# Performance work log

Measured on AMD Instinct MI355X. Metric: run time of the kernel, lower is better.

## Reference

```python
import jax, jax.numpy as jnp
import numpy as np

Q_DIM = 512
K_DIM = 512
V_DIM = 512
H_DIM = 256
B, Q, K = 4, 512, 512


def setup_inputs() -> dict:
    key = jax.random.key(0)
    ks = jax.random.split(key, 7)
    q = jax.random.normal(ks[0], (B, Q, Q_DIM), dtype=jnp.float32)
    k = jax.random.normal(ks[1], (B, K, K_DIM), dtype=jnp.float32)
    v = jax.random.normal(ks[2], (B, K, V_DIM), dtype=jnp.float32)
    S = jax.random.randint(ks[3], (B,), 1, K + 1, dtype=jnp.int64)
    # learned params (nn.Linear stores weight of shape (out, in); y = x @ W.T)
    Wq = jax.random.normal(ks[4], (H_DIM, Q_DIM), dtype=jnp.float32) / np.sqrt(Q_DIM)
    Wk = jax.random.normal(ks[5], (H_DIM, K_DIM), dtype=jnp.float32) / np.sqrt(K_DIM)
    w = jax.random.normal(ks[6], (H_DIM,), dtype=jnp.float32) / np.sqrt(H_DIM)
    return {"q": q, "k": k, "v": v, "S": S, "Wq": Wq, "Wk": Wk, "w": w}


def reference(q, k, v, S, Wq, Wk, w):
    # Additive (Bahdanau) attention scores.
    pq = jnp.einsum('bqd,hd->bqh', q, Wq)            # (B, Q, H)
    pk = jnp.einsum('bkd,hd->bkh', k, Wk)            # (B, K, H)
    t = jnp.tanh(pq[:, :, None, :] + pk[:, None, :, :])  # (B, Q, K, H)
    scores = jnp.einsum('bqkh,h->bqk', t, w)         # (B, Q, K)
    # mask keys with index >= S[b] to -inf
    kv_idx = jnp.arange(scores.shape[-1])            # (K,)
    mask = kv_idx[None, None, :] >= S[:, None, None] # (B, 1, K) -> broadcast
    scores = jnp.where(mask, -jnp.inf, scores)
    return scores
```

## Files before the change

### kernel.cpp

```cpp
#include <hip/hip_runtime.h>
#include <hip/hip_bf16.h>
#include <math.h>

#define QDIM 512
#define HDIM 256
#define QQ 512
#define KKE 512

#define TWO_LOG2E 2.8853900817779268f
#define MASK_VAL -1.0e30f

typedef __attribute__((ext_vector_type(8))) short bf16x8;
typedef __attribute__((ext_vector_type(4))) float f32x4;

__device__ __forceinline__ unsigned int pk2(float x, float y) {
  __hip_bfloat162 h = __float22bfloat162_rn(make_float2(x, y));
  unsigned int u;
  __builtin_memcpy(&u, &h, 4);
  return u;
}

__global__ __launch_bounds__(512) void proj_kernel(
    const float* __restrict__ qin, const float* __restrict__ kin,
    const float* __restrict__ Wq, const float* __restrict__ Wk,
    const float* __restrict__ wvec,
    float* __restrict__ EqT, unsigned short* __restrict__ EkT,
    float* __restrict__ wsum_out) {
  __shared__ __align__(16) unsigned short As[32 * 72];
  __shared__ __align__(16) unsigned short Bs[64 * 72];

  const int tid = threadIdx.x;
  const int lane = tid & 63;
  const int wv = __builtin_amdgcn_readfirstlane(tid >> 6);
  const int quad = lane >> 4;
  const int l16 = lane & 15;

  const int m0 = blockIdx.x * 32;
  const int h0 = blockIdx.y * 64;
  const bool isk = (blockIdx.z != 0);
  const float* A = isk ? kin : qin;
  const float* W = isk ? Wk : Wq;

  const int srow = tid >> 4;
  const int sg = (tid & 15) * 4;

  const float* arow_g = &A[(size_t)(m0 + srow) * QDIM + sg];
  const float* brow0_g = &W[(size_t)(h0 + srow) * QDIM + sg];
  const float* brow1_g = &W[(size_t)(h0 + srow + 32) * QDIM + sg];
  unsigned short* adst = &As[srow * 72 + sg];
  unsigned short* bdst0 = &Bs[srow * 72 + sg];
  unsigned short* bdst1 = &Bs[(srow + 32) * 72 + sg];

  const unsigned short* afrag = &As[((wv & 1) * 16 + l16) * 72 + quad * 8];
  const unsigned short* bfrag = &Bs[((wv >> 1) * 16 + l16) * 72 + quad * 8];

  f32x4 acc = (f32x4){0.f, 0.f, 0.f, 0.f};

  float4 pa = *(const float4*)arow_g;
  float4 pb0 = *(const float4*)brow0_g;
  float4 pb1 = *(const float4*)brow1_g;

  for (int kc = 0; kc < QDIM; kc += 64) {
    __syncthreads();
    *(uint2*)adst = make_uint2(pk2(pa.x, pa.y), pk2(pa.z, pa.w));
    *(uint2*)bdst0 = make_uint2(pk2(pb0.x, pb0.y), pk2(pb0.z, pb0.w));
    *(uint2*)bdst1 = make_uint2(pk2(pb1.x, pb1.y), pk2(pb1.z, pb1.w));
    if (kc + 64 < QDIM) {
      pa = *(const float4*)(arow_g + kc + 64);
      pb0 = *(const float4*)(brow0_g + kc + 64);
      pb1 = *(const float4*)(brow1_g + kc + 64);
    }
    __syncthreads();
    bf16x8 a0 = *(const bf16x8*)afrag;
    bf16x8 a1 = *(const bf16x8*)(afrag + 32);
    bf16x8 b0 = *(const bf16x8*)bfrag;
    bf16x8 b1 = *(const bf16x8*)(bfrag + 32);
    acc = __builtin_amdgcn_mfma_f32_16x16x32_bf16(a0, b0, acc, 0, 0, 0);
    acc = __builtin_amdgcn_mfma_f32_16x16x32_bf16(a1, b1, acc, 0, 0, 0);
  }

  const int b = m0 >> 9;
  const int hrow = h0 + (wv >> 1) * 16 + l16;
  const int mcol = (m0 & 511) + (wv & 1) * 16 + quad * 4;
  float e0 = __builtin_amdgcn_exp2f(acc[0] * TWO_LOG2E);
  float e1 = __builtin_amdgcn_exp2f(acc[1] * TWO_LOG2E);
  float e2 = __builtin_amdgcn_exp2f(acc[2] * TWO_LOG2E);
  float e3 = __builtin_amdgcn_exp2f(acc[3] * TWO_LOG2E);
  if (!isk) {
    *(float4*)(EqT + ((size_t)b * HDIM + hrow) * 512 + mcol) =
        make_float4(e0, e1, e2, e3);
    if (m0 == 0 && h0 == 0 && tid < 64) {
      float s = wvec[tid] + wvec[tid + 64] + wvec[tid + 128] + wvec[tid + 192];
#pragma unroll
      for (int off = 32; off; off >>= 1) s += __shfl_down(s, off);
      if (tid == 0) wsum_out[0] = s;
    }
  } else {
    *(uint2*)(EkT + ((size_t)b * HDIM + hrow) * 512 + mcol) =
        make_uint2(pk2(e0, e1), pk2(e2, e3));
  }
}

__global__ __launch_bounds__(256) void score_kernel(
    const float* __restrict__ EqT, const unsigned short* __restrict__ EkT,
    const float* __restrict__ wvec, const float* __restrict__ wsump,
    const int* __restrict__ Sraw, float* __restrict__ out) {
  const int b = blockIdx.z;
  const int q0 = blockIdx.y * 16;
  const int i = blockIdx.x;
  const int S = (Sraw[1] == 0) ? Sraw[2 * b] : Sraw[b];
  const int tid = threadIdx.x;
  const int wv = __builtin_amdgcn_readfirstlane(tid >> 6);
  const int L = tid & 63;
  const int q = L >> 2;
  const int k8 = (L & 3) * 8;

  __shared__ float wl[HDIM];
  __shared__ float Eqs[256][16];
  __shared__ unsigned short Eks[256][32];
  __shared__ float Cmb[3][64][8];
  wl[tid] = wvec[tid];

  const float wsum = wsump[0];
  const float* EqB = EqT + (size_t)b * (HDIM * QQ) + q0;
  const unsigned short* EkB0 = EkT + (size_t)b * (HDIM * KKE);

#pragma unroll
  for (int t = 0; t < 2; ++t) {
    const int kt = t ? (15 - i) : i;
    const int k0 = kt * 32;
    float* orow = out + ((size_t)(b * QQ + q0 + q) * KKE + k0 + k8);

    if (k0 >= S) {
      if (wv == 0) {
        float4 m4 = make_float4(MASK_VAL, MASK_VAL, MASK_VAL, MASK_VAL);
        *(float4*)&orow[0] = m4;
        *(float4*)&orow[4] = m4;
      }
      continue;
    }

    __syncthreads();
    {
      const unsigned short* EkB = EkB0 + k0;
      const int hr = tid >> 2;
      const int cq = (tid & 3) * 4;
      const int ce = (tid & 3) * 8;
#pragma unroll
      for (int p = 0; p < 4; p++) {
        *(float4*)&Eqs[hr + p * 64][cq] =
            *(const float4*)&EqB[(size_t)(hr + p * 64) * QQ + cq];
        *(uint4*)&Eks[hr + p * 64][ce] =
            *(const uint4*)&EkB[(size_t)(hr + p * 64) * KKE + ce];
      }
    }
    __syncthreads();

    float a0 = 0.f, a1 = 0.f, a2 = 0.f, a3 = 0.f;
    float a4 = 0.f, a5 = 0.f, a6 = 0.f, a7 = 0.f;
    const int hbase = wv * 64;
#pragma unroll 4
    for (int hh = 0; hh < 64; hh++) {
      const int h = hbase + hh;
      float wh = wl[h];
      float eq = Eqs[h][q];
      uint4 u = *(const uint4*)&Eks[h][k8];
      float e0 = __uint_as_float(u.x << 16);
      float e1 = __uint_as_float(u.x & 0xffff0000u);
      float e2 = __uint_as_float(u.y << 16);
      float e3 = __uint_as_float(u.y & 0xffff0000u);
      float e4 = __uint_as_float(u.z << 16);
      float e5 = __uint_as_float(u.z & 0xffff0000u);
      float e6 = __uint_as_float(u.w << 16);
      float e7 = __uint_as_float(u.w & 0xffff0000u);
      a0 = fmaf(wh, __builtin_amdgcn_rcpf(fmaf(eq, e0, 1.f)), a0);
      a1 = fmaf(wh, __builtin_amdgcn_rcpf(fmaf(eq, e1, 1.f)), a1);
      a2 = fmaf(wh, __builtin_amdgcn_rcpf(fmaf(eq, e2, 1.f)), a2);
      a3 = fmaf(wh, __builtin_amdgcn_rcpf(fmaf(eq, e3, 1.f)), a3);
      a4 = fmaf(wh, __builtin_amdgcn_rcpf(fmaf(eq, e4, 1.f)), a4);
      a5 = fmaf(wh, __builtin_amdgcn_rcpf(fmaf(eq, e5, 1.f)), a5);
      a6 = fmaf(wh, __builtin_amdgcn_rcpf(fmaf(eq, e6, 1.f)), a6);
      a7 = fmaf(wh, __builtin_amdgcn_rcpf(fmaf(eq, e7, 1.f)), a7);
    }

    if (wv > 0) {
      Cmb[wv - 1][L][0] = a0; Cmb[wv - 1][L][1] = a1;
      Cmb[wv - 1][L][2] = a2; Cmb[wv - 1][L][3] = a3;
      Cmb[wv - 1][L][4] = a4; Cmb[wv - 1][L][5] = a5;
      Cmb[wv - 1][L][6] = a6; Cmb[wv - 1][L][7] = a7;
    }
    __syncthreads();
    if (wv == 0) {
#pragma unroll
      for (int c = 0; c < 3; c++) {
        a0 += Cmb[c][L][0]; a1 += Cmb[c][L][1];
        a2 += Cmb[c][L][2]; a3 += Cmb[c][L][3];
        a4 += Cmb[c][L][4]; a5 += Cmb[c][L][5];
        a6 += Cmb[c][L][6]; a7 += Cmb[c][L][7];
      }
      const int kb = k0 + k8;
      float4 r0, r1;
      r0.x = (kb + 0 < S) ? (wsum - 2.f * a0) : MASK_VAL;
      r0.y = (kb + 1 < S) ? (wsum - 2.f * a1) : MASK_VAL;
      r0.z = (kb + 2 < S) ? (wsum - 2.f * a2) : MASK_VAL;
      r0.w = (kb + 3 < S) ? (wsum - 2.f * a3) : MASK_VAL;
      r1.x = (kb + 4 < S) ? (wsum - 2.f * a4) : MASK_VAL;
      r1.y = (kb + 5 < S) ? (wsum - 2.f * a5) : MASK_VAL;
      r1.z = (kb + 6 < S) ? (wsum - 2.f * a6) : MASK_VAL;
      r1.w = (kb + 7 < S) ? (wsum - 2.f * a7) : MASK_VAL;
      *(float4*)&orow[0] = r0;
      *(float4*)&orow[4] = r1;
    }
  }
}

extern "C" void kernel_launch(void* const* d_in, const int* in_sizes, int n_in,
                              void* d_out, int out_size, void* d_ws, size_t ws_size,
                              hipStream_t stream) {
  const float* q  = (const float*)d_in[0];
  const float* k  = (const float*)d_in[1];
  const int*   S  = (const int*)d_in[3];
  const float* Wq = (const float*)d_in[4];
  const float* Wk = (const float*)d_in[5];
  const float* w  = (const float*)d_in[6];
  float* out = (float*)d_out;

  float* wsf = (float*)d_ws;
  float* EqT = wsf;
  unsigned short* EkT = (unsigned short*)(wsf + 524288);
  float* wsum = wsf + 524288 + 262144;

  proj_kernel<<<dim3(64, 4, 2), 512, 0, stream>>>(q, k, Wq, Wk, w, EqT, EkT, wsum);
  score_kernel<<<dim3(8, 32, 4), 256, 0, stream>>>(EqT, EkT, w, wsum, S, out);
}
```

Measured before the change: 97.82 us.

## Double-buffer projection LDS tiles and hoist Eq tile load in score kernel

Result: no change. 98.35 us (+0.5%).

```diff
diff --git a/kernel.cpp b/kernel.cpp
--- a/kernel.cpp
+++ b/kernel.cpp
@@ -26,8 +26,8 @@
     const float* __restrict__ wvec,
     float* __restrict__ EqT, unsigned short* __restrict__ EkT,
     float* __restrict__ wsum_out) {
-  __shared__ __align__(16) unsigned short As[32 * 72];
-  __shared__ __align__(16) unsigned short Bs[64 * 72];
+  __shared__ __align__(16) unsigned short As[2][32 * 72];
+  __shared__ __align__(16) unsigned short Bs[2][64 * 72];
 
   const int tid = threadIdx.x;
   const int lane = tid & 63;
@@ -47,36 +47,44 @@
   const float* arow_g = &A[(size_t)(m0 + srow) * QDIM + sg];
   const float* brow0_g = &W[(size_t)(h0 + srow) * QDIM + sg];
   const float* brow1_g = &W[(size_t)(h0 + srow + 32) * QDIM + sg];
-  unsigned short* adst = &As[srow * 72 + sg];
-  unsigned short* bdst0 = &Bs[srow * 72 + sg];
-  unsigned short* bdst1 = &Bs[(srow + 32) * 72 + sg];
-
-  const unsigned short* afrag = &As[((wv & 1) * 16 + l16) * 72 + quad * 8];
-  const unsigned short* bfrag = &Bs[((wv >> 1) * 16 + l16) * 72 + quad * 8];
+  const int adst = srow * 72 + sg;
+  const int bdst0 = srow * 72 + sg;
+  const int bdst1 = (srow + 32) * 72 + sg;
+
+  const int afo = ((wv & 1) * 16 + l16) * 72 + quad * 8;
+  const int bfo = ((wv >> 1) * 16 + l16) * 72 + quad * 8;
 
   f32x4 acc = (f32x4){0.f, 0.f, 0.f, 0.f};
 
   float4 pa = *(const float4*)arow_g;
   float4 pb0 = *(const float4*)brow0_g;
   float4 pb1 = *(const float4*)brow1_g;
-
+  *(uint2*)&As[0][adst] = make_uint2(pk2(pa.x, pa.y), pk2(pa.z, pa.w));
+  *(uint2*)&Bs[0][bdst0] = make_uint2(pk2(pb0.x, pb0.y), pk2(pb0.z, pb0.w));
+  *(uint2*)&Bs[0][bdst1] = make_uint2(pk2(pb1.x, pb1.y), pk2(pb1.z, pb1.w));
+  __syncthreads();
+
+#pragma unroll
   for (int kc = 0; kc < QDIM; kc += 64) {
-    __syncthreads();
-    *(uint2*)adst = make_uint2(pk2(pa.x, pa.y), pk2(pa.z, pa.w));
-    *(uint2*)bdst0 = make_uint2(pk2(pb0.x, pb0.y), pk2(pb0.z, pb0.w));
-    *(uint2*)bdst1 = make_uint2(pk2(pb1.x, pb1.y), pk2(pb1.z, pb1.w));
-    if (kc + 64 < QDIM) {
+    const int p = (kc >> 6) & 1;
+    const bool more = (kc + 64 < QDIM);
+    if (more) {
       pa = *(const float4*)(arow_g + kc + 64);
       pb0 = *(const float4*)(brow0_g + kc + 64);
       pb1 = *(const float4*)(brow1_g + kc + 64);
     }
-    __syncthreads();
-    bf16x8 a0 = *(const bf16x8*)afrag;
-    bf16x8 a1 = *(const bf16x8*)(afrag + 32);
-    bf16x8 b0 = *(const bf16x8*)bfrag;
-    bf16x8 b1 = *(const bf16x8*)(bfrag + 32);
+    bf16x8 a0 = *(const bf16x8*)&As[p][afo];
+    bf16x8 a1 = *(const bf16x8*)&As[p][afo + 32];
+    bf16x8 b0 = *(const bf16x8*)&Bs[p][bfo];
+    bf16x8 b1 = *(const bf16x8*)&Bs[p][bfo + 32];
     acc = __builtin_amdgcn_mfma_f32_16x16x32_bf16(a0, b0, acc, 0, 0, 0);
     acc = __builtin_amdgcn_mfma_f32_16x16x32_bf16(a1, b1, acc, 0, 0, 0);
+    if (more) {
+      *(uint2*)&As[p ^ 1][adst] = make_uint2(pk2(pa.x, pa.y), pk2(pa.z, pa.w));
+      *(uint2*)&Bs[p ^ 1][bdst0] = make_uint2(pk2(pb0.x, pb0.y), pk2(pb0.z, pb0.w));
+      *(uint2*)&Bs[p ^ 1][bdst1] = make_uint2(pk2(pb1.x, pb1.y), pk2(pb1.z, pb1.w));
+    }
+    __syncthreads();
   }
 
   const int b = m0 >> 9;
@@ -101,7 +109,7 @@
   }
 }
 
-__global__ __launch_bounds__(256) void score_kernel(
+__global__ __launch_bounds__(256, 4) void score_kernel(
     const float* __restrict__ EqT, const unsigned short* __restrict__ EkT,
     const float* __restrict__ wvec, const float* __restrict__ wsump,
     const int* __restrict__ Sraw, float* __restrict__ out) {
@@ -115,54 +123,51 @@
   const int q = L >> 2;
   const int k8 = (L & 3) * 8;
 
-  __shared__ float wl[HDIM];
-  __shared__ float Eqs[256][16];
-  __shared__ unsigned short Eks[256][32];
+  __shared__ float Eqs[HDIM][16];
+  __shared__ unsigned short Eks[HDIM][32];
   __shared__ float Cmb[3][64][8];
-  wl[tid] = wvec[tid];
-
+
+  {
+    const float* src = EqT + ((size_t)b * HDIM + tid) * QQ + q0;
+    *(float4*)&Eqs[tid][0] = *(const float4*)(src + 0);
+    *(float4*)&Eqs[tid][4] = *(const float4*)(src + 4);
+    *(float4*)&Eqs[tid][8] = *(const float4*)(src + 8);
+    *(float4*)&Eqs[tid][12] = *(const float4*)(src + 12);
+  }
   const float wsum = wsump[0];
-  const float* EqB = EqT + (size_t)b * (HDIM * QQ) + q0;
-  const unsigned short* EkB0 = EkT + (size_t)b * (HDIM * KKE);
+  const unsigned short* EkB = EkT + (size_t)b * (HDIM * KKE);
+  const int hbase = wv * 64;
 
 #pragma unroll
   for (int t = 0; t < 2; ++t) {
-    const int kt = t ? (15 - i) : i;
-    const int k0 = kt * 32;
-    float* orow = out + ((size_t)(b * QQ + q0 + q) * KKE + k0 + k8);
+    const int k0 = (t ? (15 - i) : i) * 32;
+    float* op = out + ((size_t)(b * QQ + q0 + q) * KKE + k0 + k8);
 
     if (k0 >= S) {
       if (wv == 0) {
         float4 m4 = make_float4(MASK_VAL, MASK_VAL, MASK_VAL, MASK_VAL);
-        *(float4*)&orow[0] = m4;
-        *(float4*)&orow[4] = m4;
+        *(float4*)&op[0] = m4;
+        *(float4*)&op[4] = m4;
       }
       continue;
     }
 
     __syncthreads();
     {
-      const unsigned short* EkB = EkB0 + k0;
-      const int hr = tid >> 2;
-      const int cq = (tid & 3) * 4;
-      const int ce = (tid & 3) * 8;
-#pragma unroll
-      for (int p = 0; p < 4; p++) {
-        *(float4*)&Eqs[hr + p * 64][cq] =
-            *(const float4*)&EqB[(size_t)(hr + p * 64) * QQ + cq];
-        *(uint4*)&Eks[hr + p * 64][ce] =
-            *(const uint4*)&EkB[(size_t)(hr + p * 64) * KKE + ce];
-      }
+      const unsigned short* sk = EkB + (size_t)tid * KKE + k0;
+      *(uint4*)&Eks[tid][0] = *(const uint4*)(sk + 0);
+      *(uint4*)&Eks[tid][8] = *(const uint4*)(sk + 8);
+      *(uint4*)&Eks[tid][16] = *(const uint4*)(sk + 16);
+      *(uint4*)&Eks[tid][24] = *(const uint4*)(sk + 24);
     }
     __syncthreads();
 
     float a0 = 0.f, a1 = 0.f, a2 = 0.f, a3 = 0.f;
     float a4 = 0.f, a5 = 0.f, a6 = 0.f, a7 = 0.f;
-    const int hbase = wv * 64;
 #pragma unroll 4
-    for (int hh = 0; hh < 64; hh++) {
+    for (int hh = 0; hh < 64; ++hh) {
       const int h = hbase + hh;
-      float wh = wl[h];
+      float wh = wvec[h];
       float eq = Eqs[h][q];
       uint4 u = *(const uint4*)&Eks[h][k8];
       float e0 = __uint_as_float(u.x << 16);
@@ -184,19 +189,17 @@
     }
 
     if (wv > 0) {
-      Cmb[wv - 1][L][0] = a0; Cmb[wv - 1][L][1] = a1;
-      Cmb[wv - 1][L][2] = a2; Cmb[wv - 1][L][3] = a3;
-      Cmb[wv - 1][L][4] = a4; Cmb[wv - 1][L][5] = a5;
-      Cmb[wv - 1][L][6] = a6; Cmb[wv - 1][L][7] = a7;
+      *(float4*)&Cmb[wv - 1][L][0] = make_float4(a0, a1, a2, a3);
+      *(float4*)&Cmb[wv - 1][L][4] = make_float4(a4, a5, a6, a7);
     }
     __syncthreads();
     if (wv == 0) {
 #pragma unroll
       for (int c = 0; c < 3; c++) {
-        a0 += Cmb[c][L][0]; a1 += Cmb[c][L][1];
-        a2 += Cmb[c][L][2]; a3 += Cmb[c][L][3];
-        a4 += Cmb[c][L][4]; a5 += Cmb[c][L][5];
-        a6 += Cmb[c][L][6]; a7 += Cmb[c][L][7];
+        float4 x0 = *(const float4*)&Cmb[c][L][0];
+        float4 x1 = *(const float4*)&Cmb[c][L][4];
+        a0 += x0.x; a1 += x0.y; a2 += x0.z; a3 += x0.w;
+        a4 += x1.x; a5 += x1.y; a6 += x1.z; a7 += x1.w;
       }
       const int kb = k0 + k8;
       float4 r0, r1;
@@ -208,8 +211,8 @@
       r1.y = (kb + 5 < S) ? (wsum - 2.f * a5) : MASK_VAL;
       r1.z = (kb + 6 < S) ? (wsum - 2.f * a6) : MASK_VAL;
       r1.w = (kb + 7 < S) ? (wsum - 2.f * a7) : MASK_VAL;
-      *(float4*)&orow[0] = r0;
-      *(float4*)&orow[4] = r1;
+      *(float4*)&op[0] = r0;
+      *(float4*)&op[4] = r1;
     }
   }
 }
```
